# Kernel tuning notes

Hardware: AMD Instinct MI355X
Metric: run time of the kernel (lower is better)

## Reference

```python
import jax, jax.numpy as jnp
import numpy as np

HEADS = 4
ATTN_MODE = 'strided'
LOCAL_ATTN_CTX = 32
BLOCKSIZE = 32


def strided_transpose(x, n_ctx, local_attn_ctx):
    # [n, t, e] -> [n, bT_ctx, local, e] -> [n, local, bT_ctx, e] -> [n, t, e]
    bT_ctx = n_ctx // local_attn_ctx
    n, t, e = x.shape
    x = x.reshape(n, bT_ctx, local_attn_ctx, e)
    x = jnp.transpose(x, (0, 2, 1, 3))
    return x.reshape(n, t, e)


def setup_inputs() -> dict:
    key = jax.random.key(0)
    kq, kk, kv = jax.random.split(key, 3)
    shape = (2, 4096, 1024)
    return {
        'q': jax.random.normal(kq, shape, dtype=jnp.float32),
        'k': jax.random.normal(kk, shape, dtype=jnp.float32),
        'v': jax.random.normal(kv, shape, dtype=jnp.float32),
    }


def reference(q, k, v):
    n_ctx = q.shape[1]
    if ATTN_MODE == 'strided':
        bT_ctx = n_ctx // LOCAL_ATTN_CTX
        assert bT_ctx % BLOCKSIZE == 0
        q = strided_transpose(q, n_ctx, LOCAL_ATTN_CTX)
        k = strided_transpose(k, n_ctx, LOCAL_ATTN_CTX)
        v = strided_transpose(v, n_ctx, LOCAL_ATTN_CTX)
    n_state = q.shape[-1] // HEADS
    scale = 1.0 / np.sqrt(n_state)
    w = jnp.einsum('nte,nse->nts', q, k)            # [n, t, t] full scores
    w = jax.nn.softmax(w * scale, axis=-1)
    a = jnp.einsum('nts,nse->nte', w, v)
    if ATTN_MODE == 'strided':
        n, t, e = a.shape
        bT_ctx = n_ctx // LOCAL_ATTN_CTX
        a = a.reshape(n, LOCAL_ATTN_CTX, bT_ctx, e)
        a = jnp.transpose(a, (0, 2, 1, 3))
        a = a.reshape(n, t, e)
    return a
```

## Files before the change

kernel.cpp:

```cpp
#include <hip/hip_runtime.h>

using short8  = __attribute__((ext_vector_type(8))) short;
using ushort8 = __attribute__((ext_vector_type(8))) unsigned short;
using f32x4   = __attribute__((ext_vector_type(4))) float;

#define T 4096
#define E 1024
#define NB 2
#define BM 128
#define BN 128
#define BK 32
#define TILE_ELEMS (BM * BK)

__device__ __forceinline__ unsigned short f2bf(float f) {
    unsigned int u = __builtin_bit_cast(unsigned int, f);
    u = (u + 0x7FFFu + ((u >> 16) & 1u)) >> 16;
    return (unsigned short)u;
}
__device__ __forceinline__ float bf2f(unsigned short h) {
    unsigned int u = ((unsigned int)h) << 16;
    return __builtin_bit_cast(float, u);
}

__device__ __forceinline__ void gld16(const unsigned short* g, unsigned short* l) {
    __builtin_amdgcn_global_load_lds(
        (__attribute__((address_space(1))) void*)g,
        (__attribute__((address_space(3))) void*)l, 16, 0, 0);
}

__global__ __launch_bounds__(256) void prologue(const float* __restrict__ q,
                                                const float* __restrict__ k,
                                                unsigned short* __restrict__ qb,
                                                unsigned short* __restrict__ kb,
                                                float* __restrict__ lsum) {
    int bid = blockIdx.x;
    if (bid < 8192) {
        const float* src = (bid < 4096) ? q : k;
        unsigned short* dst = (bid < 4096) ? qb : kb;
        size_t i = ((size_t)(bid & 4095) * 256 + threadIdx.x) * 8;
        float4 f0 = *(const float4*)(src + i);
        float4 f1 = *(const float4*)(src + i + 4);
        ushort8 u;
        u[0]=f2bf(f0.x); u[1]=f2bf(f0.y); u[2]=f2bf(f0.z); u[3]=f2bf(f0.w);
        u[4]=f2bf(f1.x); u[5]=f2bf(f1.y); u[6]=f2bf(f1.z); u[7]=f2bf(f1.w);
        *(ushort8*)(dst + i) = u;
    } else {
        lsum[(bid - 8192) * 256 + threadIdx.x] = 0.0f;
    }
}

__global__ __launch_bounds__(256) void v_transpose(const float* __restrict__ v,
                                                   unsigned short* __restrict__ vt) {
    __shared__ float tile[64][65];
    int id  = blockIdx.x;
    int b   = id / (64 * 16);
    int rem = id % (64 * 16);
    int t0  = (rem / 16) * 64;
    int e0  = (rem % 16) * 64;
    int tid = threadIdx.x;
    int r   = tid >> 2;
    int c0  = (tid & 3) * 16;
    const float* src = v + ((size_t)(b * T + t0 + r)) * E + e0 + c0;
    #pragma unroll
    for (int i = 0; i < 4; i++) {
        float4 f = *(const float4*)(src + i * 4);
        tile[r][c0 + i*4 + 0] = f.x;
        tile[r][c0 + i*4 + 1] = f.y;
        tile[r][c0 + i*4 + 2] = f.z;
        tile[r][c0 + i*4 + 3] = f.w;
    }
    __syncthreads();
    int er = tid >> 2;
    #pragma unroll
    for (int ch = 0; ch < 2; ch++) {
        int tl = (tid & 3) * 16 + ch * 8;
        ushort8 u;
        #pragma unroll
        for (int j = 0; j < 8; j++) u[j] = f2bf(tile[tl + j][er]);
        *(ushort8*)(vt + ((size_t)(b * E + e0 + er)) * T + t0 + tl) = u;
    }
}

template <int KITERS, int NBUF>
__device__ __forceinline__ void gemm_core(const unsigned short* Abase, int apitch,
                                          const unsigned short* Bbase, int bpitch,
                                          unsigned short* ldsA, unsigned short* ldsB,
                                          int tid, f32x4 (&acc)[4][4]) {
    constexpr int D = NBUF - 1;
    const int lane = tid & 63, wave = tid >> 6;
    const int l15 = lane & 15, kq = lane >> 4;
    const int wm = (wave & 1) * 64, wn = (wave >> 1) * 64;

    const unsigned short* ga[2];
    const unsigned short* gb[2];
    int lo[2];
    #pragma unroll
    for (int i = 0; i < 2; i++) {
        int p = i * 256 + tid;
        int r = p >> 2;
        int kqw = (p & 3) ^ ((p >> 3) & 3);
        ga[i] = Abase + (size_t)r * apitch + kqw * 8;
        gb[i] = Bbase + (size_t)r * bpitch + kqw * 8;
        lo[i] = (i * 256 + wave * 64) * 8;
    }
    int aoff[4], boff[4];
    #pragma unroll
    for (int mi = 0; mi < 4; mi++) {
        int r = wm + mi * 16 + l15;
        aoff[mi] = (r * 4 + (kq ^ ((r >> 1) & 3))) * 8;
        int rn = wn + mi * 16 + l15;
        boff[mi] = (rn * 4 + (kq ^ ((rn >> 1) & 3))) * 8;
    }

    #pragma unroll
    for (int i = 0; i < D; i++) {
        gld16(ga[0] + i * BK, ldsA + i * TILE_ELEMS + lo[0]);
        gld16(ga[1] + i * BK, ldsA + i * TILE_ELEMS + lo[1]);
        gld16(gb[0] + i * BK, ldsB + i * TILE_ELEMS + lo[0]);
        gld16(gb[1] + i * BK, ldsB + i * TILE_ELEMS + lo[1]);
    }

    int cbuf = 0, pbuf = D, pkt = D;
    for (int kt = 0; kt < KITERS; kt++) {
        asm volatile("s_barrier" ::: "memory");
        gld16(ga[0] + pkt * BK, ldsA + pbuf * TILE_ELEMS + lo[0]);
        gld16(ga[1] + pkt * BK, ldsA + pbuf * TILE_ELEMS + lo[1]);
        gld16(gb[0] + pkt * BK, ldsB + pbuf * TILE_ELEMS + lo[0]);
        gld16(gb[1] + pkt * BK, ldsB + pbuf * TILE_ELEMS + lo[1]);
        if constexpr (D == 1) asm volatile("s_waitcnt vmcnt(4)" ::: "memory");
        else                  asm volatile("s_waitcnt vmcnt(8)" ::: "memory");
        asm volatile("s_barrier" ::: "memory");

        const unsigned short* A = ldsA + cbuf * TILE_ELEMS;
        const unsigned short* B = ldsB + cbuf * TILE_ELEMS;
        short8 af[4], bf[4];
        #pragma unroll
        for (int i = 0; i < 4; i++) {
            af[i] = *(const short8*)(A + aoff[i]);
            bf[i] = *(const short8*)(B + boff[i]);
        }
        #pragma unroll
        for (int mi = 0; mi < 4; mi++)
            #pragma unroll
            for (int ni = 0; ni < 4; ni++)
                acc[mi][ni] = __builtin_amdgcn_mfma_f32_16x16x32_bf16(af[mi], bf[ni], acc[mi][ni], 0, 0, 0);

        if (++cbuf == NBUF) cbuf = 0;
        if (++pbuf == NBUF) pbuf = 0;
        if (++pkt == KITERS) pkt = 0;
    }
}

__global__ __launch_bounds__(256, 2) void pass1(const unsigned short* __restrict__ qb,
                                                const unsigned short* __restrict__ kb,
                                                unsigned short* __restrict__ P,
                                                float* __restrict__ lsum) {
    __shared__ unsigned short ldsA[2 * TILE_ELEMS];
    __shared__ unsigned short ldsB[2 * TILE_ELEMS];
    const int bx = blockIdx.x;
    const int x = bx & 7, j = bx >> 3;
    const int gm = x * 8 + (j & 7);
    const int nt = j >> 3;
    const int b = gm >> 5, mt = gm & 31;
    const int tid = threadIdx.x;

    f32x4 acc[4][4];
    #pragma unroll
    for (int i = 0; i < 4; i++)
        #pragma unroll
        for (int jj = 0; jj < 4; jj++) acc[i][jj] = {};

    gemm_core<E / BK, 2>(qb + ((size_t)b * T + mt * BM) * E, E,
                         kb + ((size_t)b * T + nt * BN) * E, E,
                         ldsA, ldsB, tid, acc);

    const int lane = tid & 63, wave = tid >> 6;
    const int wm = (wave & 1) * 64, wn = (wave >> 1) * 64;
    const int quad = lane >> 4, l15 = lane & 15;
    const float sl2 = 0.0625f * 1.44269504089f;
    const int col0 = nt * BN + wn + l15;

    #pragma unroll
    for (int mi = 0; mi < 4; mi++) {
        #pragma unroll
        for (int r = 0; r < 4; r++) {
            int row = mt * BM + wm + mi * 16 + quad * 4 + r;
            size_t base = ((size_t)b * T + row) * T + col0;
            float s = 0.0f;
            #pragma unroll
            for (int ni = 0; ni < 4; ni++) {
                float p = exp2f(acc[mi][ni][r] * sl2 - 12.0f);
                unsigned short h = f2bf(p);
                P[base + ni * 16] = h;
                s += bf2f(h);
            }
            s += __shfl_xor(s, 1);
            s += __shfl_xor(s, 2);
            s += __shfl_xor(s, 4);
            s += __shfl_xor(s, 8);
            if (l15 == 0) atomicAdd(lsum + b * T + row, s);
        }
    }
}

__global__ __launch_bounds__(256, 2) void pass2(const unsigned short* __restrict__ P,
                                                const unsigned short* __restrict__ vt,
                                                const float* __restrict__ lsum,
                                                float* __restrict__ out) {
    __shared__ unsigned short ldsA[3 * TILE_ELEMS];
    __shared__ unsigned short ldsB[3 * TILE_ELEMS];
    const int bx = blockIdx.x;
    const int x = bx & 7, j = bx >> 3;
    const int gm = x * 8 + (j & 7);
    const int nt = j >> 3;
    const int b = gm >> 5, mt = gm & 31;
    const int tid = threadIdx.x;

    f32x4 acc[4][4];
    #pragma unroll
    for (int i = 0; i < 4; i++)
        #pragma unroll
        for (int jj = 0; jj < 4; jj++) acc[i][jj] = {};

    gemm_core<T / BK, 3>(P + ((size_t)b * T + mt * BM) * T, T,
                         vt + ((size_t)b * E + nt * BN) * T, T,
                         ldsA, ldsB, tid, acc);

    const int lane = tid & 63, wave = tid >> 6;
    const int wm = (wave & 1) * 64, wn = (wave >> 1) * 64;
    const int quad = lane >> 4, l15 = lane & 15;
    const int col0 = nt * BN + wn + l15;

    #pragma unroll
    for (int mi = 0; mi < 4; mi++) {
        #pragma unroll
        for (int r = 0; r < 4; r++) {
            int row = mt * BM + wm + mi * 16 + quad * 4 + r;
            float rl = 1.0f / lsum[b * T + row];
            size_t base = ((size_t)b * T + row) * E + col0;
            #pragma unroll
            for (int ni = 0; ni < 4; ni++)
                out[base + ni * 16] = acc[mi][ni][r] * rl;
        }
    }
}

extern "C" void kernel_launch(void* const* d_in, const int* in_sizes, int n_in,
                              void* d_out, int out_size, void* d_ws, size_t ws_size,
                              hipStream_t stream) {
    const float* q = (const float*)d_in[0];
    const float* k = (const float*)d_in[1];
    const float* v = (const float*)d_in[2];
    float* out = (float*)d_out;

    float* lsum = (float*)d_ws;
    unsigned short* qbw = (unsigned short*)((char*)d_ws + 32768);
    unsigned short* kbw = qbw + (size_t)NB * T * E;
    unsigned short* Pw  = kbw + (size_t)NB * T * E;
    unsigned short* vtw = qbw;

    prologue<<<8224, 256, 0, stream>>>(q, k, qbw, kbw, lsum);
    pass1<<<NB * 32 * 32, 256, 0, stream>>>(qbw, kbw, Pw, lsum);
    v_transpose<<<NB * 64 * 16, 256, 0, stream>>>(v, vtw);
    pass2<<<NB * 32 * 8, 256, 0, stream>>>(Pw, vtw, lsum, out);
}
```

Measured before the change: 313.0 us.

## Fuse V transpose into prep kernel, triple-buffer pass1, sum unrounded probabilities

Merges the Q/K bf16 conversion, the V transpose and the lsum zeroing into one prep kernel when the workspace is large enough, with V^T stored in its own buffer instead of aliasing Q. This removes one kernel launch and lets the V work overlap with the conversions. pass1 moves from two to three LDS buffers, trading LDS space for deeper prefetch. The row sum now uses the fp32 probability instead of the bf16-rounded value, which drops a conversion but makes the normaliser slightly inconsistent with the stored P.

```diff
diff --git a/kernel.cpp b/kernel.cpp
--- a/kernel.cpp
+++ b/kernel.cpp
@@ -17,10 +17,6 @@
     u = (u + 0x7FFFu + ((u >> 16) & 1u)) >> 16;
     return (unsigned short)u;
 }
-__device__ __forceinline__ float bf2f(unsigned short h) {
-    unsigned int u = ((unsigned int)h) << 16;
-    return __builtin_bit_cast(float, u);
-}
 
 __device__ __forceinline__ void gld16(const unsigned short* g, unsigned short* l) {
     __builtin_amdgcn_global_load_lds(
@@ -28,31 +24,20 @@
         (__attribute__((address_space(3))) void*)l, 16, 0, 0);
 }
 
-__global__ __launch_bounds__(256) void prologue(const float* __restrict__ q,
-                                                const float* __restrict__ k,
-                                                unsigned short* __restrict__ qb,
-                                                unsigned short* __restrict__ kb,
-                                                float* __restrict__ lsum) {
-    int bid = blockIdx.x;
-    if (bid < 8192) {
-        const float* src = (bid < 4096) ? q : k;
-        unsigned short* dst = (bid < 4096) ? qb : kb;
-        size_t i = ((size_t)(bid & 4095) * 256 + threadIdx.x) * 8;
-        float4 f0 = *(const float4*)(src + i);
-        float4 f1 = *(const float4*)(src + i + 4);
-        ushort8 u;
-        u[0]=f2bf(f0.x); u[1]=f2bf(f0.y); u[2]=f2bf(f0.z); u[3]=f2bf(f0.w);
-        u[4]=f2bf(f1.x); u[5]=f2bf(f1.y); u[6]=f2bf(f1.z); u[7]=f2bf(f1.w);
-        *(ushort8*)(dst + i) = u;
-    } else {
-        lsum[(bid - 8192) * 256 + threadIdx.x] = 0.0f;
-    }
-}
-
-__global__ __launch_bounds__(256) void v_transpose(const float* __restrict__ v,
-                                                   unsigned short* __restrict__ vt) {
-    __shared__ float tile[64][65];
-    int id  = blockIdx.x;
+__device__ __forceinline__ void do_cvt(const float* __restrict__ src,
+                                       unsigned short* __restrict__ dst, int blk) {
+    size_t i = ((size_t)blk * 256 + threadIdx.x) * 8;
+    float4 f0 = *(const float4*)(src + i);
+    float4 f1 = *(const float4*)(src + i + 4);
+    ushort8 u;
+    u[0]=f2bf(f0.x); u[1]=f2bf(f0.y); u[2]=f2bf(f0.z); u[3]=f2bf(f0.w);
+    u[4]=f2bf(f1.x); u[5]=f2bf(f1.y); u[6]=f2bf(f1.z); u[7]=f2bf(f1.w);
+    *(ushort8*)(dst + i) = u;
+}
+
+__device__ __forceinline__ void do_vt(const float* __restrict__ v,
+                                      unsigned short* __restrict__ vt, int id,
+                                      float (*tile)[65]) {
     int b   = id / (64 * 16);
     int rem = id % (64 * 16);
     int t0  = (rem / 16) * 64;
@@ -79,6 +64,37 @@
         for (int j = 0; j < 8; j++) u[j] = f2bf(tile[tl + j][er]);
         *(ushort8*)(vt + ((size_t)(b * E + e0 + er)) * T + t0 + tl) = u;
     }
+}
+
+__global__ __launch_bounds__(256) void prep(const float* __restrict__ q,
+                                            const float* __restrict__ k,
+                                            const float* __restrict__ v,
+                                            unsigned short* __restrict__ qb,
+                                            unsigned short* __restrict__ kb,
+                                            unsigned short* __restrict__ vt,
+                                            float* __restrict__ lsum) {
+    __shared__ float tile[64][65];
+    int bid = blockIdx.x;
+    if (bid < 4096)        do_cvt(q, qb, bid);
+    else if (bid < 8192)   do_cvt(k, kb, bid - 4096);
+    else if (bid < 10240)  do_vt(v, vt, bid - 8192, tile);
+    else                   lsum[(bid - 10240) * 256 + threadIdx.x] = 0.0f;
+}
+
+__global__ __launch_bounds__(256) void prologue(const float* __restrict__ q,
+                                                const float* __restrict__ k,
+                                                unsigned short* __restrict__ qb,
+                                                unsigned short* __restrict__ kb,
+                                                float* __restrict__ lsum) {
+    int bid = blockIdx.x;
+    if (bid < 4096)      do_cvt(q, qb, bid);
+    else if (bid < 8192) do_cvt(k, kb, bid - 4096);
+    else                 lsum[(bid - 8192) * 256 + threadIdx.x] = 0.0f;
+}
+__global__ __launch_bounds__(256) void v_transpose(const float* __restrict__ v,
+                                                   unsigned short* __restrict__ vt) {
+    __shared__ float tile[64][65];
+    do_vt(v, vt, blockIdx.x, tile);
 }
 
 template <int KITERS, int NBUF>
@@ -155,8 +171,8 @@
                                                 const unsigned short* __restrict__ kb,
                                                 unsigned short* __restrict__ P,
                                                 float* __restrict__ lsum) {
-    __shared__ unsigned short ldsA[2 * TILE_ELEMS];
-    __shared__ unsigned short ldsB[2 * TILE_ELEMS];
+    __shared__ unsigned short ldsA[3 * TILE_ELEMS];
+    __shared__ unsigned short ldsB[3 * TILE_ELEMS];
     const int bx = blockIdx.x;
     const int x = bx & 7, j = bx >> 3;
     const int gm = x * 8 + (j & 7);
@@ -170,7 +186,7 @@
         #pragma unroll
         for (int jj = 0; jj < 4; jj++) acc[i][jj] = {};
 
-    gemm_core<E / BK, 2>(qb + ((size_t)b * T + mt * BM) * E, E,
+    gemm_core<E / BK, 3>(qb + ((size_t)b * T + mt * BM) * E, E,
                          kb + ((size_t)b * T + nt * BN) * E, E,
                          ldsA, ldsB, tid, acc);
 
@@ -190,9 +206,8 @@
             #pragma unroll
             for (int ni = 0; ni < 4; ni++) {
                 float p = exp2f(acc[mi][ni][r] * sl2 - 12.0f);
-                unsigned short h = f2bf(p);
-                P[base + ni * 16] = h;
-                s += bf2f(h);
+                P[base + ni * 16] = f2bf(p);
+                s += p;
             }
             s += __shfl_xor(s, 1);
             s += __shfl_xor(s, 2);
@@ -253,14 +268,25 @@
     const float* v = (const float*)d_in[2];
     float* out = (float*)d_out;
 
+    const size_t QK = (size_t)NB * T * E;
+    const size_t PSZ = (size_t)NB * T * T;
     float* lsum = (float*)d_ws;
     unsigned short* qbw = (unsigned short*)((char*)d_ws + 32768);
-    unsigned short* kbw = qbw + (size_t)NB * T * E;
-    unsigned short* Pw  = kbw + (size_t)NB * T * E;
-    unsigned short* vtw = qbw;
-
-    prologue<<<8224, 256, 0, stream>>>(q, k, qbw, kbw, lsum);
-    pass1<<<NB * 32 * 32, 256, 0, stream>>>(qbw, kbw, Pw, lsum);
-    v_transpose<<<NB * 64 * 16, 256, 0, stream>>>(v, vtw);
-    pass2<<<NB * 32 * 8, 256, 0, stream>>>(Pw, vtw, lsum, out);
-}
+    unsigned short* kbw = qbw + QK;
+    unsigned short* Pw  = kbw + QK;
+
+    const size_t full_need = 32768 + (3 * QK + PSZ) * sizeof(unsigned short);
+
+    if (ws_size >= full_need) {
+        unsigned short* vtw = Pw + PSZ;
+        prep<<<10272, 256, 0, stream>>>(q, k, v, qbw, kbw, vtw, lsum);
+        pass1<<<NB * 32 * 32, 256, 0, stream>>>(qbw, kbw, Pw, lsum);
+        pass2<<<NB * 32 * 8, 256, 0, stream>>>(Pw, vtw, lsum, out);
+    } else {
+        unsigned short* vtw = qbw;
+        prologue<<<8224, 256, 0, stream>>>(q, k, qbw, kbw, lsum);
+        pass1<<<NB * 32 * 32, 256, 0, stream>>>(qbw, kbw, Pw, lsum);
+        v_transpose<<<NB * 64 * 16, 256, 0, stream>>>(v, vtw);
+        pass2<<<NB * 32 * 8, 256, 0, stream>>>(Pw, vtw, lsum, out);
+    }
+}
```

Result: no change. 308.1 us (-1.6%).
